# Performance work log

Measured on AMD Instinct MI355X. Metric: run time of the kernel, lower is better.

## Reference

```python
import jax, jax.numpy as jnp
import numpy as np


def setup_inputs() -> dict:
    key = jax.random.key(0)
    k1, k2, k3, k4, k5 = jax.random.split(key, 5)
    N, IN, OUT = 4096, 2048, 2048
    return {
        "input": jax.random.normal(k1, (N, IN), dtype=jnp.float32),
        "weight_mu": jax.random.normal(k2, (OUT, IN), dtype=jnp.float32) * 0.25,
        "weight_rho": jax.random.normal(k3, (OUT, IN), dtype=jnp.float32) - 5.0,
        "eps_weight": jax.random.normal(k4, (OUT, IN), dtype=jnp.float32),
        "bias": jax.random.normal(k5, (OUT,), dtype=jnp.float32) * 0.02,
    }


def reference(input, weight_mu, weight_rho, eps_weight, bias):
    # Effective weight: mu + softplus(rho) * eps   (log1p(exp(rho)) == softplus)
    w = weight_mu + jax.nn.softplus(weight_rho) * eps_weight  # [out, in]
    # F.linear: input @ w.T + bias
    return jnp.einsum("ni,oi->no", input, w) + bias
```

## Files before the change

kernel.cpp:

```cpp
#include <hip/hip_runtime.h>
#include <stdint.h>

typedef __bf16 bf16x8 __attribute__((ext_vector_type(8)));
typedef float f32x4 __attribute__((ext_vector_type(4)));
typedef float float4v __attribute__((ext_vector_type(4)));
typedef unsigned short u16x8 __attribute__((ext_vector_type(8)));

__device__ __forceinline__ unsigned short f2bf(float f) {
    unsigned u = __float_as_uint(f);
    u += 0x7fffu + ((u >> 16) & 1u);
    return (unsigned short)(u >> 16);
}

__device__ __forceinline__ float softplus(float x) {
    return fmaxf(x, 0.0f) + __logf(1.0f + __expf(-fabsf(x)));
}

__device__ __forceinline__ void gl_lds16(const void* gptr, void* lptr) {
    auto g = reinterpret_cast<const __attribute__((address_space(1))) void*>(
        reinterpret_cast<uintptr_t>(gptr));
    auto l = reinterpret_cast<__attribute__((address_space(3))) void*>(
        reinterpret_cast<uintptr_t>(lptr));
    __builtin_amdgcn_global_load_lds(g, l, 16, 0, 0);
}

__global__ void prep_kernel(const float* __restrict__ in,
                            const float* __restrict__ mu,
                            const float* __restrict__ rho,
                            const float* __restrict__ eps,
                            unsigned short* __restrict__ in_bf,
                            unsigned short* __restrict__ w_bf,
                            int nIn8, int nW8) {
    int i = blockIdx.x * blockDim.x + threadIdx.x;
    if (i < nIn8) {
        const float4v* p = (const float4v*)in + (size_t)i * 2;
        float4v a = p[0], b = p[1];
        u16x8 r;
        r[0] = f2bf(a[0]); r[1] = f2bf(a[1]); r[2] = f2bf(a[2]); r[3] = f2bf(a[3]);
        r[4] = f2bf(b[0]); r[5] = f2bf(b[1]); r[6] = f2bf(b[2]); r[7] = f2bf(b[3]);
        ((u16x8*)in_bf)[i] = r;
    } else {
        int j = i - nIn8;
        if (j >= nW8) return;
        const float4v* pm = (const float4v*)mu  + (size_t)j * 2;
        const float4v* pr = (const float4v*)rho + (size_t)j * 2;
        const float4v* pe = (const float4v*)eps + (size_t)j * 2;
        float4v m0 = pm[0], m1 = pm[1];
        float4v r0 = pr[0], r1 = pr[1];
        float4v e0 = pe[0], e1 = pe[1];
        u16x8 r;
        r[0] = f2bf(m0[0] + softplus(r0[0]) * e0[0]);
        r[1] = f2bf(m0[1] + softplus(r0[1]) * e0[1]);
        r[2] = f2bf(m0[2] + softplus(r0[2]) * e0[2]);
        r[3] = f2bf(m0[3] + softplus(r0[3]) * e0[3]);
        r[4] = f2bf(m1[0] + softplus(r1[0]) * e1[0]);
        r[5] = f2bf(m1[1] + softplus(r1[1]) * e1[1]);
        r[6] = f2bf(m1[2] + softplus(r1[2]) * e1[2]);
        r[7] = f2bf(m1[3] + softplus(r1[3]) * e1[3]);
        ((u16x8*)w_bf)[j] = r;
    }
}

#define BM 128
#define BN 128
#define KC 32
#define SLOT_U 8192

__global__ __launch_bounds__(256, 2)
void gemm_bt_kernel(const unsigned short* __restrict__ A,
                    const unsigned short* __restrict__ B,
                    const float* __restrict__ bias,
                    float* __restrict__ C,
                    int M, int N, int K) {
    __shared__ unsigned short lds[4][SLOT_U];

    const int t      = threadIdx.x;
    const int lane   = t & 63;
    const int wave   = t >> 6;
    const int lane16 = lane & 15;
    const int quad   = lane >> 4;
    const int wm     = wave & 1;
    const int wn     = wave >> 1;

    const int m0 = blockIdx.y * BM;
    const int n0 = blockIdx.x * BN;

    const int r   = t >> 2;
    const int key = (t >> 3) & 3;
    const int kgs = ((t & 3) ^ key) * 8;

    const unsigned short* a0 = A + (size_t)(m0 + r)      * K + kgs;
    const unsigned short* a1 = A + (size_t)(m0 + 64 + r) * K + kgs;
    const unsigned short* b0 = B + (size_t)(n0 + r)      * K + kgs;
    const unsigned short* b1 = B + (size_t)(n0 + 64 + r) * K + kgs;

    f32x4 acc[4][4] = {};

    auto stage = [&](int slot, int kc) {
        const int k0 = kc * KC;
        gl_lds16(a0 + k0, &lds[slot][t * 8]);
        gl_lds16(a1 + k0, &lds[slot][2048 + t * 8]);
        gl_lds16(b0 + k0, &lds[slot][4096 + t * 8]);
        gl_lds16(b1 + k0, &lds[slot][6144 + t * 8]);
    };

    const int nchunk = K / KC;
    stage(0, 0);
    stage(1, 1);
    stage(2, 2);

    const int sw = (lane16 >> 1) & 3;
    const int ra = (wm * 64 + lane16) * KC + ((quad ^ sw) * 8);
    const int rb = 4096 + (wn * 64 + lane16) * KC + ((quad ^ sw) * 8);

#pragma unroll 4
    for (int i = 0; i < nchunk; ++i) {
        const int slot = i & 3;
        stage((i + 3) & 3, (i + 3 < nchunk) ? (i + 3) : (nchunk - 1));
        asm volatile("s_waitcnt vmcnt(12)" ::: "memory");
        __builtin_amdgcn_sched_barrier(0);
        __builtin_amdgcn_s_barrier();
        const unsigned short* ls = lds[slot];
        bf16x8 af[4], bf[4];
#pragma unroll
        for (int mi = 0; mi < 4; ++mi)
            af[mi] = *(const bf16x8*)(ls + ra + mi * 16 * KC);
#pragma unroll
        for (int ni = 0; ni < 4; ++ni)
            bf[ni] = *(const bf16x8*)(ls + rb + ni * 16 * KC);
        __builtin_amdgcn_s_setprio(1);
#pragma unroll
        for (int mi = 0; mi < 4; ++mi)
#pragma unroll
            for (int ni = 0; ni < 4; ++ni)
                acc[mi][ni] = __builtin_amdgcn_mfma_f32_16x16x32_bf16(
                    af[mi], bf[ni], acc[mi][ni], 0, 0, 0);
        __builtin_amdgcn_s_setprio(0);
        asm volatile("s_waitcnt lgkmcnt(0)" ::: "memory");
        __builtin_amdgcn_sched_barrier(0);
        __builtin_amdgcn_s_barrier();
    }

    float bv[4];
#pragma unroll
    for (int ni = 0; ni < 4; ++ni)
        bv[ni] = bias[n0 + wn * 64 + ni * 16 + lane16];

#pragma unroll
    for (int mi = 0; mi < 4; ++mi) {
        const int rbase = m0 + wm * 64 + mi * 16 + quad * 4;
#pragma unroll
        for (int ni = 0; ni < 4; ++ni) {
            const int col = n0 + wn * 64 + ni * 16 + lane16;
#pragma unroll
            for (int rr = 0; rr < 4; ++rr)
                C[(size_t)(rbase + rr) * N + col] = acc[mi][ni][rr] + bv[ni];
        }
    }
}

extern "C" void kernel_launch(void* const* d_in, const int* in_sizes, int n_in,
                              void* d_out, int out_size, void* d_ws, size_t ws_size,
                              hipStream_t stream) {
    const float* input = (const float*)d_in[0];
    const float* mu    = (const float*)d_in[1];
    const float* rho   = (const float*)d_in[2];
    const float* eps   = (const float*)d_in[3];
    const float* bias  = (const float*)d_in[4];
    float* out = (float*)d_out;

    const int OUT = in_sizes[4];
    const int IN  = in_sizes[1] / OUT;
    const int M   = in_sizes[0] / IN;

    unsigned short* in_bf = (unsigned short*)d_ws;
    unsigned short* w_bf  = in_bf + (size_t)M * IN;

    const int nIn8 = (M * IN) / 8;
    const int nW8  = (OUT * IN) / 8;
    prep_kernel<<<dim3((nIn8 + nW8 + 255) / 256), 256, 0, stream>>>(
        input, mu, rho, eps, in_bf, w_bf, nIn8, nW8);

    gemm_bt_kernel<<<dim3(OUT / BN, M / BM), 256, 0, stream>>>(
        in_bf, w_bf, bias, out, M, OUT, IN);
}
```

Measured before the change: 165.9 us.

## Double-buffer LDS fragment registers to overlap reads with MFMA

The GEMM main loop now keeps two register sets of A/B fragments, loading the next chunk's fragments from LDS while issuing MFMAs on the current ones. The loop is unrolled by two with swapped buffers and one barrier per iteration instead of two. This aims to hide LDS read latency behind matrix math and cut synchronization, at the cost of more VGPRs, which could hurt occupancy under the 2-block launch bound. The slot-reuse timing with a single barrier relies on the wait counts being right.

```diff
diff --git a/kernel.cpp b/kernel.cpp
--- a/kernel.cpp
+++ b/kernel.cpp
@@ -105,41 +105,63 @@
     };
 
     const int nchunk = K / KC;
+
+    const int sw = (lane16 >> 1) & 3;
+    const int ra = (wm * 64 + lane16) * KC + ((quad ^ sw) * 8);
+    const int rb = 4096 + (wn * 64 + lane16) * KC + ((quad ^ sw) * 8);
+
+    bf16x8 fA[2][4], fB[2][4];
+
     stage(0, 0);
     stage(1, 1);
     stage(2, 2);
-
-    const int sw = (lane16 >> 1) & 3;
-    const int ra = (wm * 64 + lane16) * KC + ((quad ^ sw) * 8);
-    const int rb = 4096 + (wn * 64 + lane16) * KC + ((quad ^ sw) * 8);
-
-#pragma unroll 4
-    for (int i = 0; i < nchunk; ++i) {
-        const int slot = i & 3;
-        stage((i + 3) & 3, (i + 3 < nchunk) ? (i + 3) : (nchunk - 1));
-        asm volatile("s_waitcnt vmcnt(12)" ::: "memory");
-        __builtin_amdgcn_sched_barrier(0);
-        __builtin_amdgcn_s_barrier();
-        const unsigned short* ls = lds[slot];
-        bf16x8 af[4], bf[4];
+    asm volatile("s_waitcnt vmcnt(8)" ::: "memory");
+    __builtin_amdgcn_sched_barrier(0);
+    __builtin_amdgcn_s_barrier();
+    __builtin_amdgcn_sched_barrier(0);
+    {
+        const unsigned short* ls0 = lds[0];
 #pragma unroll
         for (int mi = 0; mi < 4; ++mi)
-            af[mi] = *(const bf16x8*)(ls + ra + mi * 16 * KC);
+            fA[0][mi] = *(const bf16x8*)(ls0 + ra + mi * 16 * KC);
 #pragma unroll
         for (int ni = 0; ni < 4; ++ni)
-            bf[ni] = *(const bf16x8*)(ls + rb + ni * 16 * KC);
-        __builtin_amdgcn_s_setprio(1);
-#pragma unroll
-        for (int mi = 0; mi < 4; ++mi)
-#pragma unroll
-            for (int ni = 0; ni < 4; ++ni)
-                acc[mi][ni] = __builtin_amdgcn_mfma_f32_16x16x32_bf16(
-                    af[mi], bf[ni], acc[mi][ni], 0, 0, 0);
-        __builtin_amdgcn_s_setprio(0);
-        asm volatile("s_waitcnt lgkmcnt(0)" ::: "memory");
-        __builtin_amdgcn_sched_barrier(0);
-        __builtin_amdgcn_s_barrier();
-    }
+            fB[0][ni] = *(const bf16x8*)(ls0 + rb + ni * 16 * KC);
+    }
+
+#define HALF_ITER(RD, CP, kk)                                               \
+    {                                                                       \
+        const int k_ = (kk);                                                \
+        stage((k_ + 3) & 3, (k_ + 3 < nchunk) ? (k_ + 3) : (nchunk - 1));   \
+        asm volatile("s_waitcnt vmcnt(8)" ::: "memory");                    \
+        __builtin_amdgcn_sched_barrier(0);                                  \
+        __builtin_amdgcn_s_barrier();                                       \
+        __builtin_amdgcn_sched_barrier(0);                                  \
+        const int rc_ = (k_ + 1 < nchunk) ? (k_ + 1) : (nchunk - 1);        \
+        const unsigned short* ls_ = lds[rc_ & 3];                           \
+        _Pragma("unroll")                                                   \
+        for (int mi = 0; mi < 4; ++mi)                                      \
+            fA[RD][mi] = *(const bf16x8*)(ls_ + ra + mi * 16 * KC);         \
+        _Pragma("unroll")                                                   \
+        for (int ni = 0; ni < 4; ++ni)                                      \
+            fB[RD][ni] = *(const bf16x8*)(ls_ + rb + ni * 16 * KC);         \
+        __builtin_amdgcn_s_setprio(1);                                      \
+        _Pragma("unroll")                                                   \
+        for (int mi = 0; mi < 4; ++mi)                                      \
+            _Pragma("unroll")                                               \
+            for (int ni = 0; ni < 4; ++ni)                                  \
+                acc[mi][ni] = __builtin_amdgcn_mfma_f32_16x16x32_bf16(      \
+                    fA[CP][mi], fB[CP][ni], acc[mi][ni], 0, 0, 0);          \
+        __builtin_amdgcn_s_setprio(0);                                      \
+        asm volatile("s_waitcnt lgkmcnt(0)" ::: "memory");                  \
+        __builtin_amdgcn_sched_barrier(0);                                  \
+    }
+
+    for (int k = 0; k < nchunk; k += 2) {
+        HALF_ITER(1, 0, k);
+        HALF_ITER(0, 1, k + 1);
+    }
+#undef HALF_ITER
 
     float bv[4];
 #pragma unroll
```

Result: no change. 165.8 us (-0.1%).

## Enlarge GEMM block to 256x128 with 8 waves and double-buffered LDS

Applied to the files above, without the earlier changes.

The GEMM block tile grows from 128x128 with 4 waves to 256x128 with 8 waves, so each B tile loaded into LDS is shared by twice as many rows. The 4-slot pipeline that kept three chunks in flight is replaced by a simpler 2-buffer ping-pong: the next chunk is issued after the current fragments are read, and each iteration ends with __syncthreads. This targets global/LDS traffic per FLOP, but gives up prefetch depth, so global-load latency may be exposed more and the grid has half as many blocks.

```diff
diff --git a/kernel.cpp b/kernel.cpp
--- a/kernel.cpp
+++ b/kernel.cpp
@@ -61,26 +61,26 @@
     }
 }
 
-#define BM 128
+#define BM 256
 #define BN 128
 #define KC 32
-#define SLOT_U 8192
+#define BUF_U 12288
 
-__global__ __launch_bounds__(256, 2)
+__global__ __launch_bounds__(512, 4)
 void gemm_bt_kernel(const unsigned short* __restrict__ A,
                     const unsigned short* __restrict__ B,
                     const float* __restrict__ bias,
                     float* __restrict__ C,
                     int M, int N, int K) {
-    __shared__ unsigned short lds[4][SLOT_U];
+    __shared__ unsigned short lds[2][BUF_U];
 
     const int t      = threadIdx.x;
     const int lane   = t & 63;
     const int wave   = t >> 6;
     const int lane16 = lane & 15;
     const int quad   = lane >> 4;
-    const int wm     = wave & 1;
-    const int wn     = wave >> 1;
+    const int wm     = wave & 3;
+    const int wn     = wave >> 2;
 
     const int m0 = blockIdx.y * BM;
     const int n0 = blockIdx.x * BN;
@@ -89,56 +89,51 @@
     const int key = (t >> 3) & 3;
     const int kgs = ((t & 3) ^ key) * 8;
 
-    const unsigned short* a0 = A + (size_t)(m0 + r)      * K + kgs;
-    const unsigned short* a1 = A + (size_t)(m0 + 64 + r) * K + kgs;
-    const unsigned short* b0 = B + (size_t)(n0 + r)      * K + kgs;
-    const unsigned short* b1 = B + (size_t)(n0 + 64 + r) * K + kgs;
+    const unsigned short* aP0 = A + (size_t)(m0 + r)       * K + kgs;
+    const unsigned short* aP1 = A + (size_t)(m0 + 128 + r) * K + kgs;
+    const unsigned short* bP  = B + (size_t)(n0 + r)       * K + kgs;
 
     f32x4 acc[4][4] = {};
 
-    auto stage = [&](int slot, int kc) {
-        const int k0 = kc * KC;
-        gl_lds16(a0 + k0, &lds[slot][t * 8]);
-        gl_lds16(a1 + k0, &lds[slot][2048 + t * 8]);
-        gl_lds16(b0 + k0, &lds[slot][4096 + t * 8]);
-        gl_lds16(b1 + k0, &lds[slot][6144 + t * 8]);
+    auto stage = [&](int buf, int it) {
+        const int k0 = it * KC;
+        gl_lds16(aP0 + k0, &lds[buf][t * 8]);
+        gl_lds16(aP1 + k0, &lds[buf][4096 + t * 8]);
+        gl_lds16(bP  + k0, &lds[buf][8192 + t * 8]);
     };
-
-    const int nchunk = K / KC;
-    stage(0, 0);
-    stage(1, 1);
-    stage(2, 2);
 
     const int sw = (lane16 >> 1) & 3;
     const int ra = (wm * 64 + lane16) * KC + ((quad ^ sw) * 8);
-    const int rb = 4096 + (wn * 64 + lane16) * KC + ((quad ^ sw) * 8);
+    const int rb = 8192 + (wn * 64 + lane16) * KC + ((quad ^ sw) * 8);
 
-#pragma unroll 4
-    for (int i = 0; i < nchunk; ++i) {
-        const int slot = i & 3;
-        stage((i + 3) & 3, (i + 3 < nchunk) ? (i + 3) : (nchunk - 1));
-        asm volatile("s_waitcnt vmcnt(12)" ::: "memory");
-        __builtin_amdgcn_sched_barrier(0);
-        __builtin_amdgcn_s_barrier();
-        const unsigned short* ls = lds[slot];
-        bf16x8 af[4], bf[4];
+    const int nit = K / KC;
+    stage(0, 0);
+    __syncthreads();
+
+    auto body = [&](int cur, int it) {
+        const unsigned short* la = lds[cur];
+        bf16x8 af[4], bfr[4];
 #pragma unroll
         for (int mi = 0; mi < 4; ++mi)
-            af[mi] = *(const bf16x8*)(ls + ra + mi * 16 * KC);
+            af[mi] = *(const bf16x8*)(la + ra + mi * 16 * KC);
 #pragma unroll
         for (int ni = 0; ni < 4; ++ni)
-            bf[ni] = *(const bf16x8*)(ls + rb + ni * 16 * KC);
+            bfr[ni] = *(const bf16x8*)(la + rb + ni * 16 * KC);
+        if (it + 1 < nit) stage(cur ^ 1, it + 1);
         __builtin_amdgcn_s_setprio(1);
 #pragma unroll
         for (int mi = 0; mi < 4; ++mi)
 #pragma unroll
             for (int ni = 0; ni < 4; ++ni)
                 acc[mi][ni] = __builtin_amdgcn_mfma_f32_16x16x32_bf16(
-                    af[mi], bf[ni], acc[mi][ni], 0, 0, 0);
+                    af[mi], bfr[ni], acc[mi][ni], 0, 0, 0);
         __builtin_amdgcn_s_setprio(0);
-        asm volatile("s_waitcnt lgkmcnt(0)" ::: "memory");
-        __builtin_amdgcn_sched_barrier(0);
-        __builtin_amdgcn_s_barrier();
+        __syncthreads();
+    };
+
+    for (int it = 0; it < nit; it += 2) {
+        body(0, it);
+        body(1, it + 1);
     }
 
     float bv[4];
@@ -181,6 +176,6 @@
     prep_kernel<<<dim3((nIn8 + nW8 + 255) / 256), 256, 0, stream>>>(
         input, mu, rho, eps, in_bf, w_bf, nIn8, nW8);
 
-    gemm_bt_kernel<<<dim3(OUT / BN, M / BM), 256, 0, stream>>>(
+    gemm_bt_kernel<<<dim3(OUT / BN, M / BM), 512, 0, stream>>>(
         in_bf, w_bf, bias, out, M, OUT, IN);
 }
```

After: 171.2 us. +3.2%, slower.
